# Kernel tuning notes

Measured on AMD Instinct MI355X. Metric: run time of the kernel, lower is better.

The kernel has to match this reference:

```python
import jax, jax.numpy as jnp
import numpy as np


def setup_inputs() -> dict:
    key = jax.random.key(0)
    k0, k1, k2, k3, k4 = jax.random.split(key, 5)
    B, S, D, F, E = 2, 1024, 1024, 2048, 8
    x = jax.random.normal(k0, (B, S, D), dtype=jnp.float32)
    router_weight = jax.random.normal(k1, (D, E), dtype=jnp.float32) * (1.0 / np.sqrt(D))
    std_in = (1.0 / np.sqrt(3.0)) / np.sqrt(D)   # fan_in = d_model for w1/w2
    std_out = (1.0 / np.sqrt(3.0)) / np.sqrt(F)  # fan_in = d_ff for w3
    w1 = jax.random.normal(k2, (E, D, F), dtype=jnp.float32) * std_in
    w2 = jax.random.normal(k3, (E, D, F), dtype=jnp.float32) * std_in
    w3 = jax.random.normal(k4, (E, F, D), dtype=jnp.float32) * std_out
    return {"x": x, "router_weight": router_weight, "w1": w1, "w2": w2, "w3": w3, "top_k": 2}


def reference(x, router_weight, w1, w2, w3, top_k):
    B, S, D = x.shape
    E = w1.shape[0]
    xf = x.reshape(-1, D)                         # (T, D), T = B*S
    T = xf.shape[0]
    # Router: linear + softmax + top-k, then renormalize top-k weights
    logits = xf @ router_weight                   # (T, E)
    probs = jax.nn.softmax(logits, axis=-1)
    topk_w, topk_idx = jax.lax.top_k(probs, top_k)  # (T, k)
    topk_w = topk_w / jnp.sum(topk_w, axis=-1, keepdims=True)
    # Dense combine weights: cw[t, e] = routing weight if expert e selected for token t, else 0
    cw = jnp.zeros((T, E), dtype=xf.dtype).at[jnp.arange(T)[:, None], topk_idx].add(topk_w)
    # Expert SwiGLU: loop over small fixed expert count (structurally distinct weights)
    out = jnp.zeros_like(xf)
    for e in range(E):
        h = jax.nn.silu(xf @ w1[e]) * (xf @ w2[e])  # (T, F)
        out = out + cw[:, e:e + 1] * (h @ w3[e])    # (T, D)
    return out.reshape(B, S, D)
```

## Files before the change

kernel.cpp:

```cpp
#include <hip/hip_runtime.h>
#include <hip/hip_bf16.h>
#include <stdint.h>

#define T_TOK 2048
#define DMODEL 1024
#define FDIM 2048
#define NEXP 8
#define MAXS 40
#define MAXS2 24

typedef __bf16 bf16;
typedef __attribute__((ext_vector_type(8))) __bf16 bf16x8;
typedef __attribute__((ext_vector_type(4))) float f32x4;

#define GLOBAL_AS __attribute__((address_space(1)))
#define LDS_AS __attribute__((address_space(3)))
#define VMCNT(n) asm volatile("s_waitcnt vmcnt(" #n ")" ::: "memory")
#define GLD16(src, dst) __builtin_amdgcn_global_load_lds((const GLOBAL_AS void*)(src), (LDS_AS void*)(dst), 16, 0, 0)

#define XG_SLOT   131072u
#define H_SLOT    262144u
#define W_SLAB    2097152u

__global__ __launch_bounds__(64) void moe_router(
    const float* __restrict__ x, const float* __restrict__ rw,
    bf16* __restrict__ xb, int* __restrict__ counts,
    int* __restrict__ tok_list, float* __restrict__ wgt_list)
{
  const int t = blockIdx.x;
  const int lane = threadIdx.x;
  const float* xr = x + (size_t)t * DMODEL;
  float acc[NEXP];
#pragma unroll
  for (int e = 0; e < NEXP; ++e) acc[e] = 0.f;
  for (int d = lane; d < DMODEL; d += 64) {
    float xv = xr[d];
    if (xb) xb[(size_t)t * DMODEL + d] = (bf16)xv;
    const float* r = rw + (size_t)d * NEXP;
#pragma unroll
    for (int e = 0; e < NEXP; ++e) acc[e] += xv * r[e];
  }
#pragma unroll
  for (int e = 0; e < NEXP; ++e) {
#pragma unroll
    for (int off = 32; off >= 1; off >>= 1)
      acc[e] += __shfl_xor(acc[e], off, 64);
  }
  if (lane == 0) {
    int i0 = 0; float m0 = acc[0];
#pragma unroll
    for (int e = 1; e < NEXP; ++e) { if (acc[e] > m0) { m0 = acc[e]; i0 = e; } }
    int i1 = -1; float m1 = -3.402823466e38f;
#pragma unroll
    for (int e = 0; e < NEXP; ++e) { if (e != i0 && acc[e] > m1) { m1 = acc[e]; i1 = e; } }
    float r = expf(m1 - m0);
    float w0 = 1.f / (1.f + r);
    float w1v = r / (1.f + r);
    int p0 = atomicAdd(&counts[i0], 1);
    tok_list[i0 * T_TOK + p0] = t;
    wgt_list[i0 * T_TOK + p0] = w0;
    int p1 = atomicAdd(&counts[i1], 1);
    tok_list[i1 * T_TOK + p1] = t;
    wgt_list[i1 * T_TOK + p1] = w1v;
  }
}

__global__ void moe_prefix(const int* __restrict__ counts, int* __restrict__ base,
                           int* __restrict__ sched, int* __restrict__ sched256)
{
  if (threadIdx.x == 0) {
    int sstart[NEXP];
    int s = 0, i = 0;
    for (int e = 0; e < NEXP; ++e) {
      base[e] = s; s += counts[e];
      sstart[e] = i;
      const int nt = (counts[e] + 127) / 128;
      for (int tt = 0; tt < nt; ++tt) sched[i++] = (e << 16) | tt;
    }
    for (int k = i; k < MAXS; ++k) sched[k] = -1;
    int i2 = 0;
    for (int e = 0; e < NEXP; ++e) {
      const int nt128 = (counts[e] + 127) / 128;
      const int nt256 = (counts[e] + 255) / 256;
      for (int j = 0; j < nt256; ++j) {
        const int lo = sstart[e] + 2 * j;
        const int hi = (2 * j + 1 < nt128) ? lo + 1 : lo;
        sched256[i2++] = (e << 28) | (j << 24) | (lo << 8) | hi;
      }
    }
    for (int k = i2; k < MAXS2; ++k) sched256[k] = -1;
  }
}

__global__ __launch_bounds__(256) void moe_gather(
    const float* __restrict__ x, const int* __restrict__ tok_list,
    const int* __restrict__ counts, const int* __restrict__ sched,
    bf16* __restrict__ xg)
{
  const int s = sched[blockIdx.x];
  if (s < 0) return;
  const int e = s >> 16, tt = s & 0xffff;
  int rem = counts[e] - tt * 128; if (rem > 128) rem = 128;
  const int w = threadIdx.x >> 6, lane = threadIdx.x & 63;
  const int r = blockIdx.y * 4 + w;
  const int rc = r < rem ? r : rem - 1;
  const int tok = tok_list[e * T_TOK + tt * 128 + rc];
  const float* xr = x + (size_t)tok * DMODEL + lane * 16;
  f32x4 v0 = *(const f32x4*)(xr);
  f32x4 v1 = *(const f32x4*)(xr + 4);
  f32x4 v2 = *(const f32x4*)(xr + 8);
  f32x4 v3 = *(const f32x4*)(xr + 12);
  bf16x8 a, b;
#pragma unroll
  for (int j = 0; j < 4; ++j) { a[j] = (bf16)v0[j]; a[4 + j] = (bf16)v1[j]; }
#pragma unroll
  for (int j = 0; j < 4; ++j) { b[j] = (bf16)v2[j]; b[4 + j] = (bf16)v3[j]; }
  bf16* dst = xg + (size_t)blockIdx.x * XG_SLOT + (size_t)(lane * 2) * 1024 + r * 8;
  *(bf16x8*)dst = a;
  *(bf16x8*)(dst + 1024) = b;
}

__global__ __launch_bounds__(256) void transpose_blk12(
    const float* __restrict__ w1, const float* __restrict__ w2,
    bf16* __restrict__ w1b, bf16* __restrict__ w2b)
{
  const int C = FDIM;
  __shared__ float tile[64][65];
  const int z = blockIdx.z;
  const int e = z & 7;
  const float* inp = (z < 8 ? w1 : w2) + (size_t)e * DMODEL * FDIM;
  bf16* outp = (z < 8 ? w1b : w2b) + (size_t)e * W_SLAB;
  const int rb = blockIdx.y * 64;
  const int cb = blockIdx.x * 64;
  const int tid = threadIdx.x;
  const int r = tid >> 2, c0 = (tid & 3) * 16;
  const float* src = inp + (size_t)(rb + r) * C + (cb + c0);
#pragma unroll
  for (int j = 0; j < 16; j += 4) {
    f32x4 v = *(const f32x4*)(src + j);
    tile[r][c0 + j + 0] = v[0];
    tile[r][c0 + j + 1] = v[1];
    tile[r][c0 + j + 2] = v[2];
    tile[r][c0 + j + 3] = v[3];
  }
  __syncthreads();
  bf16x8 a, b;
#pragma unroll
  for (int j = 0; j < 8; ++j) a[j] = (bf16)tile[c0 + j][r];
#pragma unroll
  for (int j = 0; j < 8; ++j) b[j] = (bf16)tile[c0 + 8 + j][r];
  const int ft = blockIdx.x;
  const int ktd = blockIdx.y * 2 + c0 / 32;
  const int kc = (c0 & 31) / 8;
  bf16* dst = outp + ((size_t)ft * 128 + ktd * 4 + kc) * 512 + r * 8;
  *(bf16x8*)dst = a;
  *(bf16x8*)(dst + 512) = b;
}

__global__ __launch_bounds__(256) void transpose_blk3(
    const float* __restrict__ w3, bf16* __restrict__ w3b)
{
  const int C = DMODEL;
  __shared__ float tile[64][65];
  const int e = blockIdx.z;
  const float* inp = w3 + (size_t)e * FDIM * DMODEL;
  bf16* outp = w3b + (size_t)e * W_SLAB;
  const int rb = blockIdx.y * 64;
  const int cb = blockIdx.x * 64;
  const int tid = threadIdx.x;
  const int r = tid >> 2, c0 = (tid & 3) * 16;
  const float* src = inp + (size_t)(rb + r) * C + (cb + c0);
#pragma unroll
  for (int j = 0; j < 16; j += 4) {
    f32x4 v = *(const f32x4*)(src + j);
    tile[r][c0 + j + 0] = v[0];
    tile[r][c0 + j + 1] = v[1];
    tile[r][c0 + j + 2] = v[2];
    tile[r][c0 + j + 3] = v[3];
  }
  __syncthreads();
  bf16x8 a, b;
#pragma unroll
  for (int j = 0; j < 8; ++j) a[j] = (bf16)tile[c0 + j][r];
#pragma unroll
  for (int j = 0; j < 8; ++j) b[j] = (bf16)tile[c0 + 8 + j][r];
  const int dt = blockIdx.x;
  const int ktf = blockIdx.y * 2 + c0 / 32;
  const int kc = (c0 & 31) / 8;
  bf16* dst = outp + ((size_t)dt * 256 + ktf * 4 + kc) * 512 + r * 8;
  *(bf16x8*)dst = a;
  *(bf16x8*)(dst + 512) = b;
}

__global__ __launch_bounds__(512) void moe_gemm1_blk(
    const bf16* __restrict__ xg,
    const bf16* __restrict__ w1b, const bf16* __restrict__ w2b,
    const int* __restrict__ counts, const int* __restrict__ sched256,
    bf16* __restrict__ hblk)
{
  const int s = sched256[blockIdx.y];
  if (s < 0) return;
  const int e = (s >> 28) & 7, t256 = (s >> 24) & 15;
  const int sLo = (s >> 8) & 0xff, sHi = s & 0xff;
  int rem = counts[e] - t256 * 256; if (rem > 256) rem = 256;
  const int ft = blockIdx.x;

  __shared__ __align__(16) bf16 As[3][4][256][8];
  __shared__ __align__(16) bf16 Ws[3][2][4][64][8];

  const int tid = threadIdx.x;
  const int lane = tid & 63;
  const int w = tid >> 6;
  const int wr = w >> 1, wc = w & 1;
  const int lh = lane >> 4, ll = lane & 15;

  const int c0 = 2 * w, c1 = 2 * w + 1;
  const int kc0 = c0 >> 2, q0 = c0 & 3;
  const int kc1 = c1 >> 2, q1 = c1 & 3;
  const bf16* asrc0 = xg + (size_t)(q0 >= 2 ? sHi : sLo) * XG_SLOT + kc0 * 1024 + (q0 & 1) * 512 + lane * 8;
  const bf16* asrc1 = xg + (size_t)(q1 >= 2 ? sHi : sLo) * XG_SLOT + kc1 * 1024 + (q1 & 1) * 512 + lane * 8;
  const int wm = w >> 2, wkc = w & 3;
  const bf16* wsrc = (wm ? w2b : w1b) + (size_t)e * W_SLAB + ((size_t)ft * 128 + wkc) * 512 + lane * 8;

  f32x4 acc1[4][2], acc2[4][2];
  const f32x4 fz = {0.f, 0.f, 0.f, 0.f};
#pragma unroll
  for (int mf = 0; mf < 4; ++mf)
#pragma unroll
    for (int nf = 0; nf < 2; ++nf) { acc1[mf][nf] = fz; acc2[mf][nf] = fz; }

#define STAGE1(B, KT)                                              \
  {                                                                \
    GLD16(asrc0 + (size_t)(KT) * 4096, &As[B][kc0][q0 * 64][0]);   \
    GLD16(asrc1 + (size_t)(KT) * 4096, &As[B][kc1][q1 * 64][0]);   \
    GLD16(wsrc  + (size_t)(KT) * 2048, &Ws[B][wm][wkc][0][0]);     \
  }

  const int NT = DMODEL / 32;
  STAGE1(0, 0);
  STAGE1(1, 1);
  VMCNT(3);
  __builtin_amdgcn_s_barrier();

  int ld = 0;
  for (int t = 0; t < NT; ++t) {
    int pf = ld + 2; if (pf >= 3) pf -= 3;
    if (t + 2 < NT) STAGE1(pf, t + 2);

    bf16x8 af[4], b1[2], b2[2];
#pragma unroll
    for (int mf = 0; mf < 4; ++mf)
      af[mf] = *(const bf16x8*)&As[ld][lh][wr * 64 + mf * 16 + ll][0];
#pragma unroll
    for (int nf = 0; nf < 2; ++nf) {
      b1[nf] = *(const bf16x8*)&Ws[ld][0][lh][wc * 32 + nf * 16 + ll][0];
      b2[nf] = *(const bf16x8*)&Ws[ld][1][lh][wc * 32 + nf * 16 + ll][0];
    }
    __builtin_amdgcn_s_setprio(1);
#pragma unroll
    for (int mf = 0; mf < 4; ++mf)
#pragma unroll
      for (int nf = 0; nf < 2; ++nf) {
        acc1[mf][nf] = __builtin_amdgcn_mfma_f32_16x16x32_bf16(af[mf], b1[nf], acc1[mf][nf], 0, 0, 0);
        acc2[mf][nf] = __builtin_amdgcn_mfma_f32_16x16x32_bf16(af[mf], b2[nf], acc2[mf][nf], 0, 0, 0);
      }
    __builtin_amdgcn_s_setprio(0);

    if (t + 2 < NT)      { VMCNT(3); __builtin_amdgcn_s_barrier(); }
    else if (t + 1 < NT) { VMCNT(0); __builtin_amdgcn_s_barrier(); }
    ld = (ld + 1 == 3) ? 0 : ld + 1;
  }
#undef STAGE1

  const int kth = ft * 2 + wc;
#pragma unroll
  for (int mf = 0; mf < 4; ++mf)
#pragma unroll
    for (int nf = 0; nf < 2; ++nf) {
      const int kch = nf * 2 + (ll >> 3);
#pragma unroll
      for (int r = 0; r < 4; ++r) {
        const int rl = wr * 64 + mf * 16 + lh * 4 + r;
        if (rl < rem) {
          bf16* hs = hblk + (size_t)(rl < 128 ? sLo : sHi) * H_SLOT;
          const float a = acc1[mf][nf][r];
          const float b = acc2[mf][nf][r];
          const float h = (a / (1.f + expf(-a))) * b;
          hs[((size_t)kth * 4 + kch) * 1024 + (size_t)(rl & 127) * 8 + (ll & 7)] = (bf16)h;
        }
      }
    }
}

__global__ __launch_bounds__(256) void moe_gemm2_blk(
    const bf16* __restrict__ hblk, const bf16* __restrict__ w3b,
    const int* __restrict__ tok_list, const float* __restrict__ wgt_list,
    const int* __restrict__ counts, const int* __restrict__ sched,
    float* __restrict__ out)
{
  const int s = sched[blockIdx.y];
  if (s < 0) return;
  const int e = s >> 16, tt = s & 0xffff;
  int rem = counts[e] - tt * 128; if (rem > 128) rem = 128;
  const int dtb = blockIdx.x;
  const int kz = blockIdx.z;

  __shared__ __align__(16) bf16 As[3][4][128][8];
  __shared__ __align__(16) bf16 Ws[3][4][128][8];
  __shared__ int toks[128];
  __shared__ float wgts[128];

  const int tid = threadIdx.x;
  const int lane = tid & 63;
  const int w = tid >> 6;
  const int wr = w >> 1, wc = w & 1;
  const int lh = lane >> 4, ll = lane & 15;

  if (tid < 128) {
    int r = tid < rem ? tid : rem - 1;
    toks[tid] = tok_list[e * T_TOK + tt * 128 + r];
    wgts[tid] = wgt_list[e * T_TOK + tt * 128 + r];
  }
  __syncthreads();

  const bf16* ah = hblk + (size_t)blockIdx.y * H_SLOT + (size_t)kz * 131072 + w * 1024 + lane * 8;
  const int fh = w & 1;
  const int kcp = (w >> 1) << 1;
  const bf16* w3w = w3b + (size_t)e * W_SLAB
      + ((size_t)(2 * dtb + fh) * 256 + (size_t)kz * 128 + kcp) * 512 + lane * 8;

  f32x4 acc[4][4];
  const f32x4 fz = {0.f, 0.f, 0.f, 0.f};
#pragma unroll
  for (int mf = 0; mf < 4; ++mf)
#pragma unroll
    for (int nf = 0; nf < 4; ++nf) acc[mf][nf] = fz;

#define STAGE2(B, KT)                                                    \
  {                                                                      \
    GLD16(ah  + (size_t)(KT) * 4096,       &As[B][w][0][0]);             \
    GLD16(ah  + (size_t)(KT) * 4096 + 512, &As[B][w][64][0]);            \
    GLD16(w3w + (size_t)(KT) * 2048,       &Ws[B][kcp][fh * 64][0]);     \
    GLD16(w3w + (size_t)(KT) * 2048 + 512, &Ws[B][kcp + 1][fh * 64][0]); \
  }

  const int NT = (FDIM / 2) / 32;
  STAGE2(0, 0);
  STAGE2(1, 1);
  VMCNT(4);
  __builtin_amdgcn_s_barrier();

  int ld = 0;
  for (int t = 0; t < NT; ++t) {
    int pf = ld + 2; if (pf >= 3) pf -= 3;
    if (t + 2 < NT) STAGE2(pf, t + 2);

    bf16x8 af[4], bv[4];
#pragma unroll
    for (int mf = 0; mf < 4; ++mf)
      af[mf] = *(const bf16x8*)&As[ld][lh][wr * 64 + mf * 16 + ll][0];
#pragma unroll
    for (int nf = 0; nf < 4; ++nf)
      bv[nf] = *(const bf16x8*)&Ws[ld][lh][wc * 64 + nf * 16 + ll][0];
    __builtin_amdgcn_s_setprio(1);
#pragma unroll
    for (int mf = 0; mf < 4; ++mf)
#pragma unroll
      for (int nf = 0; nf < 4; ++nf)
        acc[mf][nf] = __builtin_amdgcn_mfma_f32_16x16x32_bf16(af[mf], bv[nf], acc[mf][nf], 0, 0, 0);
    __builtin_amdgcn_s_setprio(0);

    if (t + 2 < NT)      { VMCNT(4); __builtin_amdgcn_s_barrier(); }
    else if (t + 1 < NT) { VMCNT(0); __builtin_amdgcn_s_barrier(); }
    ld = (ld + 1 == 3) ? 0 : ld + 1;
  }
#undef STAGE2

#pragma unroll
  for (int mf = 0; mf < 4; ++mf)
#pragma unroll
    for (int nf = 0; nf < 4; ++nf)
#pragma unroll
      for (int r = 0; r < 4; ++r) {
        const int rl = wr * 64 + mf * 16 + lh * 4 + r;
        if (rl < rem) {
          const int col = dtb * 128 + wc * 64 + nf * 16 + ll;
          atomicAdd(&out[(size_t)toks[rl] * DMODEL + col], acc[mf][nf][r] * wgts[rl]);
        }
      }
}

__global__ __launch_bounds__(256, 2) void moe_gemm1(
    const bf16* __restrict__ xb,
    const float* __restrict__ w1, const float* __restrict__ w2,
    const int* __restrict__ tok_list, const int* __restrict__ counts,
    const int* __restrict__ base, bf16* __restrict__ H)
{
  const int e = blockIdx.z;
  const int tt = blockIdx.y;
  const int ft = blockIdx.x;
  const int cnt = counts[e];
  if (tt * 128 >= cnt) return;
  int rem = cnt - tt * 128; if (rem > 128) rem = 128;

  __shared__ __align__(16) bf16 As[4][128][8];
  __shared__ __align__(16) bf16 Ws[2][4][64][8];
  __shared__ int toks[128];

  const int tid = threadIdx.x;
  const int lane = tid & 63;
  const int w = tid >> 6;
  const int wr = w >> 1, wc = w & 1;
  const int lh = lane >> 4, ll = lane & 15;

  if (tid < 128) {
    int r = tid < rem ? tid : rem - 1;
    toks[tid] = tok_list[e * T_TOK + tt * 128 + r];
  }
  __syncthreads();

  f32x4 acc1[4][2], acc2[4][2];
  const f32x4 fz = {0.f, 0.f, 0.f, 0.f};
#pragma unroll
  for (int mf = 0; mf < 4; ++mf)
#pragma unroll
    for (int nf = 0; nf < 2; ++nf) { acc1[mf][nf] = fz; acc2[mf][nf] = fz; }

  const float* w1e = w1 + (size_t)e * DMODEL * FDIM + ft * 64;
  const float* w2e = w2 + (size_t)e * DMODEL * FDIM + ft * 64;
  const int sf = tid & 63;
  const int skc = tid >> 6;

  for (int k0 = 0; k0 < DMODEL; k0 += 32) {
    __syncthreads();
#pragma unroll
    for (int i = 0; i < 2; ++i) {
      const int c = w + i * 4;
      const int kc = c >> 1;
      const int rh = c & 1;
      const int row = rh * 64 + lane;
      GLD16(xb + (size_t)toks[row] * DMODEL + (k0 + kc * 8), &As[kc][rh * 64][0]);
    }
    {
      const size_t rowoff = (size_t)(k0 + skc * 8) * FDIM + sf;
      const float* s1 = w1e + rowoff;
      const float* s2 = w2e + rowoff;
      bf16x8 v1, v2;
#pragma unroll
      for (int j = 0; j < 8; ++j) {
        v1[j] = (bf16)s1[(size_t)j * FDIM];
        v2[j] = (bf16)s2[(size_t)j * FDIM];
      }
      *(bf16x8*)&Ws[0][skc][sf][0] = v1;
      *(bf16x8*)&Ws[1][skc][sf][0] = v2;
    }
    __syncthreads();
    bf16x8 af[4];
#pragma unroll
    for (int mf = 0; mf < 4; ++mf)
      af[mf] = *(const bf16x8*)&As[lh][wr * 64 + mf * 16 + ll][0];
    bf16x8 b1[2], b2[2];
#pragma unroll
    for (int nf = 0; nf < 2; ++nf) {
      b1[nf] = *(const bf16x8*)&Ws[0][lh][wc * 32 + nf * 16 + ll][0];
      b2[nf] = *(const bf16x8*)&Ws[1][lh][wc * 32 + nf * 16 + ll][0];
    }
#pragma unroll
    for (int mf = 0; mf < 4; ++mf)
#pragma unroll
      for (int nf = 0; nf < 2; ++nf) {
        acc1[mf][nf] = __builtin_amdgcn_mfma_f32_16x16x32_bf16(af[mf], b1[nf], acc1[mf][nf], 0, 0, 0);
        acc2[mf][nf] = __builtin_amdgcn_mfma_f32_16x16x32_bf16(af[mf], b2[nf], acc2[mf][nf], 0, 0, 0);
      }
  }

  const int hbase = base[e] + tt * 128;
#pragma unroll
  for (int mf = 0; mf < 4; ++mf)
#pragma unroll
    for (int nf = 0; nf < 2; ++nf)
#pragma unroll
      for (int r = 0; r < 4; ++r) {
        const int rl = wr * 64 + mf * 16 + lh * 4 + r;
        if (rl < rem) {
          const int fg = ft * 64 + wc * 32 + nf * 16 + ll;
          const float a = acc1[mf][nf][r];
          const float b = acc2[mf][nf][r];
          const float h = (a / (1.f + expf(-a))) * b;
          H[(size_t)(hbase + rl) * FDIM + fg] = (bf16)h;
        }
      }
}

__global__ __launch_bounds__(256, 2) void moe_gemm2(
    const bf16* __restrict__ H, const float* __restrict__ w3,
    const int* __restrict__ tok_list, const float* __restrict__ wgt_list,
    const int* __restrict__ counts, const int* __restrict__ base,
    float* __restrict__ out)
{
  const int e = blockIdx.z;
  const int tt = blockIdx.y;
  const int dt = blockIdx.x;
  const int cnt = counts[e];
  if (tt * 128 >= cnt) return;
  int rem = cnt - tt * 128; if (rem > 128) rem = 128;

  __shared__ __align__(16) bf16 As[4][128][8];
  __shared__ __align__(16) bf16 Ws[4][64][8];
  __shared__ int toks[128];
  __shared__ float wgts[128];

  const int tid = threadIdx.x;
  const int lane = tid & 63;
  const int w = tid >> 6;
  const int wr = w >> 1, wc = w & 1;
  const int lh = lane >> 4, ll = lane & 15;

  if (tid < 128) {
    int r = tid < rem ? tid : rem - 1;
    toks[tid] = tok_list[e * T_TOK + tt * 128 + r];
    wgts[tid] = wgt_list[e * T_TOK + tt * 128 + r];
  }
  __syncthreads();

  f32x4 acc[4][2];
  const f32x4 fz = {0.f, 0.f, 0.f, 0.f};
#pragma unroll
  for (int mf = 0; mf < 4; ++mf)
#pragma unroll
    for (int nf = 0; nf < 2; ++nf) acc[mf][nf] = fz;

  const int hbase = base[e] + tt * 128;
  const float* w3e = w3 + (size_t)e * FDIM * DMODEL + dt * 64;
  const int sf = tid & 63;
  const int skc = tid >> 6;

  for (int k0 = 0; k0 < FDIM; k0 += 32) {
    __syncthreads();
#pragma unroll
    for (int i = 0; i < 2; ++i) {
      const int c = w + i * 4;
      const int kc = c >> 1;
      const int rh = c & 1;
      int row = rh * 64 + lane;
      if (row >= rem) row = rem - 1;
      GLD16(H + (size_t)(hbase + row) * FDIM + (k0 + kc * 8), &As[kc][rh * 64][0]);
    }
    {
      const size_t rowoff = (size_t)(k0 + skc * 8) * DMODEL + sf;
      const float* s3 = w3e + rowoff;
      bf16x8 v;
#pragma unroll
      for (int j = 0; j < 8; ++j) v[j] = (bf16)s3[(size_t)j * DMODEL];
      *(bf16x8*)&Ws[skc][sf][0] = v;
    }
    __syncthreads();
    bf16x8 af[4];
#pragma unroll
    for (int mf = 0; mf < 4; ++mf)
      af[mf] = *(const bf16x8*)&As[lh][wr * 64 + mf * 16 + ll][0];
    bf16x8 bv[2];
#pragma unroll
    for (int nf = 0; nf < 2; ++nf)
      bv[nf] = *(const bf16x8*)&Ws[lh][wc * 32 + nf * 16 + ll][0];
#pragma unroll
    for (int mf = 0; mf < 4; ++mf)
#pragma unroll
      for (int nf = 0; nf < 2; ++nf)
        acc[mf][nf] = __builtin_amdgcn_mfma_f32_16x16x32_bf16(af[mf], bv[nf], acc[mf][nf], 0, 0, 0);
  }

#pragma unroll
  for (int mf = 0; mf < 4; ++mf)
#pragma unroll
    for (int nf = 0; nf < 2; ++nf)
#pragma unroll
      for (int r = 0; r < 4; ++r) {
        const int rl = wr * 64 + mf * 16 + lh * 4 + r;
        if (rl < rem) {
          const int col = dt * 64 + wc * 32 + nf * 16 + ll;
          atomicAdd(&out[(size_t)toks[rl] * DMODEL + col], acc[mf][nf][r] * wgts[rl]);
        }
      }
}

extern "C" void kernel_launch(void* const* d_in, const int* in_sizes, int n_in,
                              void* d_out, int out_size, void* d_ws, size_t ws_size,
                              hipStream_t stream)
{
  const float* x  = (const float*)d_in[0];
  const float* rw = (const float*)d_in[1];
  const float* w1 = (const float*)d_in[2];
  const float* w2 = (const float*)d_in[3];
  const float* w3 = (const float*)d_in[4];
  float* out = (float*)d_out;
  char* ws = (char*)d_ws;

  size_t off = 0;
  auto take = [&](size_t bytes) -> char* {
    char* p = ws + off;
    off = (off + bytes + 255) & ~(size_t)255;
    return p;
  };
  int* tok_list   = (int*)take((size_t)NEXP * T_TOK * sizeof(int));
  float* wgt_list = (float*)take((size_t)NEXP * T_TOK * sizeof(float));
  int* counts     = (int*)take(64);
  int* base       = (int*)take(64);
  int* sched      = (int*)take(MAXS * sizeof(int));
  int* sched256   = (int*)take(MAXS2 * sizeof(int));
  bf16* xg        = (bf16*)take((size_t)MAXS * XG_SLOT * sizeof(bf16));
  bf16* hblk      = (bf16*)take((size_t)MAXS * H_SLOT * sizeof(bf16));
  bf16* w1b       = (bf16*)take((size_t)NEXP * W_SLAB * sizeof(bf16));
  bf16* w2b       = (bf16*)take((size_t)NEXP * W_SLAB * sizeof(bf16));
  bf16* w3b       = (bf16*)take((size_t)NEXP * W_SLAB * sizeof(bf16));
  const bool fast = (ws_size >= off);

  hipMemsetAsync(d_out, 0, (size_t)out_size * sizeof(float), stream);
  hipMemsetAsync(counts, 0, NEXP * sizeof(int), stream);

  if (fast) {
    moe_router<<<dim3(T_TOK), dim3(64), 0, stream>>>(x, rw, nullptr, counts, tok_list, wgt_list);
    moe_prefix<<<dim3(1), dim3(64), 0, stream>>>(counts, base, sched, sched256);
    transpose_blk12<<<dim3(FDIM / 64, DMODEL / 64, 2 * NEXP), dim3(256), 0, stream>>>(w1, w2, w1b, w2b);
    transpose_blk3<<<dim3(DMODEL / 64, FDIM / 64, NEXP), dim3(256), 0, stream>>>(w3, w3b);
    moe_gather<<<dim3(MAXS, 32), dim3(256), 0, stream>>>(x, tok_list, counts, sched, xg);
    moe_gemm1_blk<<<dim3(FDIM / 64, MAXS2), dim3(512), 0, stream>>>(
        xg, w1b, w2b, counts, sched256, hblk);
    moe_gemm2_blk<<<dim3(DMODEL / 128, MAXS, 2), dim3(256), 0, stream>>>(
        hblk, w3b, tok_list, wgt_list, counts, sched, out);
  } else {
    size_t foff = 0;
    auto ftake = [&](size_t bytes) -> char* {
      char* p = ws + foff;
      foff = (foff + bytes + 255) & ~(size_t)255;
      return p;
    };
    int* ftok   = (int*)ftake((size_t)NEXP * T_TOK * sizeof(int));
    float* fwgt = (float*)ftake((size_t)NEXP * T_TOK * sizeof(float));
    int* fcnt   = (int*)ftake(64);
    int* fbase  = (int*)ftake(64);
    int* fsched = (int*)ftake(MAXS * sizeof(int));
    int* fs256  = (int*)ftake(MAXS2 * sizeof(int));
    bf16* xb    = (bf16*)ftake((size_t)T_TOK * DMODEL * sizeof(bf16));
    bf16* H     = (bf16*)ftake((size_t)2 * T_TOK * FDIM * sizeof(bf16));
    hipMemsetAsync(fcnt, 0, NEXP * sizeof(int), stream);
    moe_router<<<dim3(T_TOK), dim3(64), 0, stream>>>(x, rw, xb, fcnt, ftok, fwgt);
    moe_prefix<<<dim3(1), dim3(64), 0, stream>>>(fcnt, fbase, fsched, fs256);
    moe_gemm1<<<dim3(FDIM / 64, T_TOK / 128, NEXP), dim3(256), 0, stream>>>(
        xb, w1, w2, ftok, fcnt, fbase, H);
    moe_gemm2<<<dim3(DMODEL / 64, T_TOK / 128, NEXP), dim3(256), 0, stream>>>(
        H, w3, ftok, fwgt, fcnt, fbase, out);
  }
}
```

Measured before the change: 250.7 us.

## Enlarge gemm2 token tile to 256 rows with 512-thread blocks

```diff
diff --git a/kernel.cpp b/kernel.cpp
--- a/kernel.cpp
+++ b/kernel.cpp
@@ -292,23 +292,24 @@
     }
 }
 
-__global__ __launch_bounds__(256) void moe_gemm2_blk(
+__global__ __launch_bounds__(512) void moe_gemm2_blk(
     const bf16* __restrict__ hblk, const bf16* __restrict__ w3b,
     const int* __restrict__ tok_list, const float* __restrict__ wgt_list,
-    const int* __restrict__ counts, const int* __restrict__ sched,
+    const int* __restrict__ counts, const int* __restrict__ sched256,
     float* __restrict__ out)
 {
-  const int s = sched[blockIdx.y];
+  const int s = sched256[blockIdx.y];
   if (s < 0) return;
-  const int e = s >> 16, tt = s & 0xffff;
-  int rem = counts[e] - tt * 128; if (rem > 128) rem = 128;
+  const int e = (s >> 28) & 7, t256 = (s >> 24) & 15;
+  const int sLo = (s >> 8) & 0xff, sHi = s & 0xff;
+  int rem = counts[e] - t256 * 256; if (rem > 256) rem = 256;
   const int dtb = blockIdx.x;
   const int kz = blockIdx.z;
 
-  __shared__ __align__(16) bf16 As[3][4][128][8];
+  __shared__ __align__(16) bf16 As[3][4][256][8];
   __shared__ __align__(16) bf16 Ws[3][4][128][8];
-  __shared__ int toks[128];
-  __shared__ float wgts[128];
+  __shared__ int toks[256];
+  __shared__ float wgts[256];
 
   const int tid = threadIdx.x;
   const int lane = tid & 63;
@@ -316,18 +317,23 @@
   const int wr = w >> 1, wc = w & 1;
   const int lh = lane >> 4, ll = lane & 15;
 
-  if (tid < 128) {
+  if (tid < 256) {
     int r = tid < rem ? tid : rem - 1;
-    toks[tid] = tok_list[e * T_TOK + tt * 128 + r];
-    wgts[tid] = wgt_list[e * T_TOK + tt * 128 + r];
+    toks[tid] = tok_list[e * T_TOK + t256 * 256 + r];
+    wgts[tid] = wgt_list[e * T_TOK + t256 * 256 + r];
   }
   __syncthreads();
 
-  const bf16* ah = hblk + (size_t)blockIdx.y * H_SLOT + (size_t)kz * 131072 + w * 1024 + lane * 8;
-  const int fh = w & 1;
-  const int kcp = (w >> 1) << 1;
-  const bf16* w3w = w3b + (size_t)e * W_SLAB
-      + ((size_t)(2 * dtb + fh) * 256 + (size_t)kz * 128 + kcp) * 512 + lane * 8;
+  const int c0 = 2 * w, c1 = 2 * w + 1;
+  const int kc0 = c0 >> 2, q0 = c0 & 3;
+  const int kc1 = c1 >> 2, q1 = c1 & 3;
+  const bf16* asrc0 = hblk + (size_t)(q0 >= 2 ? sHi : sLo) * H_SLOT + (size_t)kz * 131072
+      + kc0 * 1024 + (q0 & 1) * 512 + lane * 8;
+  const bf16* asrc1 = hblk + (size_t)(q1 >= 2 ? sHi : sLo) * H_SLOT + (size_t)kz * 131072
+      + kc1 * 1024 + (q1 & 1) * 512 + lane * 8;
+  const int fh = w & 1, wkc = w >> 1;
+  const bf16* wsrc = w3b + (size_t)e * W_SLAB
+      + ((size_t)(2 * dtb + fh) * 256 + (size_t)kz * 128 + wkc) * 512 + lane * 8;
 
   f32x4 acc[4][4];
   const f32x4 fz = {0.f, 0.f, 0.f, 0.f};
@@ -336,18 +342,17 @@
 #pragma unroll
     for (int nf = 0; nf < 4; ++nf) acc[mf][nf] = fz;
 
-#define STAGE2(B, KT)                                                    \
-  {                                                                      \
-    GLD16(ah  + (size_t)(KT) * 4096,       &As[B][w][0][0]);             \
-    GLD16(ah  + (size_t)(KT) * 4096 + 512, &As[B][w][64][0]);            \
-    GLD16(w3w + (size_t)(KT) * 2048,       &Ws[B][kcp][fh * 64][0]);     \
-    GLD16(w3w + (size_t)(KT) * 2048 + 512, &Ws[B][kcp + 1][fh * 64][0]); \
+#define STAGE2(B, KT)                                              \
+  {                                                                \
+    GLD16(asrc0 + (size_t)(KT) * 4096, &As[B][kc0][q0 * 64][0]);   \
+    GLD16(asrc1 + (size_t)(KT) * 4096, &As[B][kc1][q1 * 64][0]);   \
+    GLD16(wsrc  + (size_t)(KT) * 2048, &Ws[B][wkc][fh * 64][0]);   \
   }
 
   const int NT = (FDIM / 2) / 32;
   STAGE2(0, 0);
   STAGE2(1, 1);
-  VMCNT(4);
+  VMCNT(3);
   __builtin_amdgcn_s_barrier();
 
   int ld = 0;
@@ -370,7 +375,7 @@
         acc[mf][nf] = __builtin_amdgcn_mfma_f32_16x16x32_bf16(af[mf], bv[nf], acc[mf][nf], 0, 0, 0);
     __builtin_amdgcn_s_setprio(0);
 
-    if (t + 2 < NT)      { VMCNT(4); __builtin_amdgcn_s_barrier(); }
+    if (t + 2 < NT)      { VMCNT(3); __builtin_amdgcn_s_barrier(); }
     else if (t + 1 < NT) { VMCNT(0); __builtin_amdgcn_s_barrier(); }
     ld = (ld + 1 == 3) ? 0 : ld + 1;
   }
@@ -626,8 +631,8 @@
     moe_gather<<<dim3(MAXS, 32), dim3(256), 0, stream>>>(x, tok_list, counts, sched, xg);
     moe_gemm1_blk<<<dim3(FDIM / 64, MAXS2), dim3(512), 0, stream>>>(
         xg, w1b, w2b, counts, sched256, hblk);
-    moe_gemm2_blk<<<dim3(DMODEL / 128, MAXS, 2), dim3(256), 0, stream>>>(
-        hblk, w3b, tok_list, wgt_list, counts, sched, out);
+    moe_gemm2_blk<<<dim3(DMODEL / 128, MAXS2, 2), dim3(512), 0, stream>>>(
+        hblk, w3b, tok_list, wgt_list, counts, sched256, out);
   } else {
     size_t foff = 0;
     auto ftake = [&](size_t bytes) -> char* {
```

Measured after the change: 250.1 us. No clear change (-0.2%).
